# Optimization experiments

Measured on AMD Instinct MI355X. Metric: run time of the kernel, lower is better.

Reference implementation:

```python
import jax, jax.numpy as jnp
import numpy as np

H = 64
N_NODES = 12000
N_EDGES = 50000


def setup_inputs() -> dict:
    key = jax.random.key(0)
    ks = jax.random.split(key, 16)
    s = 1.0 / np.sqrt(H)
    inp = {
        "node": jax.random.normal(ks[0], (N_NODES, H), jnp.float32),
        "edge": jax.random.normal(ks[1], (N_EDGES, H), jnp.float32),
        "hidden_feats": jax.random.normal(ks[2], (N_NODES, H), jnp.float32),
        "src": jax.random.randint(ks[3], (N_EDGES,), 0, N_NODES, jnp.int32),
        "dst": jax.random.randint(ks[4], (N_EDGES,), 0, N_NODES, jnp.int32),
        # edge_network: Linear(H, 2H) -> ReLU -> Linear(2H, H*H)
        "W1": jax.random.uniform(ks[5], (2 * H, H), jnp.float32, -s, s),
        "b1": jax.random.uniform(ks[6], (2 * H,), jnp.float32, -s, s),
        "W2": jax.random.uniform(ks[7], (H * H, 2 * H), jnp.float32, -1 / np.sqrt(2 * H), 1 / np.sqrt(2 * H)),
        "b2": jax.random.uniform(ks[8], (H * H,), jnp.float32, -1 / np.sqrt(2 * H), 1 / np.sqrt(2 * H)),
        # GRUCell params (torch layout: [3H, H], gate order r,z,n)
        "W_ih": jax.random.uniform(ks[9], (3 * H, H), jnp.float32, -s, s),
        "W_hh": jax.random.uniform(ks[10], (3 * H, H), jnp.float32, -s, s),
        "b_ih": jax.random.uniform(ks[11], (3 * H,), jnp.float32, -s, s),
        "b_hh": jax.random.uniform(ks[12], (3 * H,), jnp.float32, -s, s),
        # LayerNorm params
        "gamma": jnp.ones((H,), jnp.float32),
        "beta": jnp.zeros((H,), jnp.float32),
    }
    return inp


def _gru_cell(x, h, W_ih, W_hh, b_ih, b_hh):
    gi = x @ W_ih.T + b_ih  # [N, 3H]
    gh = h @ W_hh.T + b_hh  # [N, 3H]
    r = jax.nn.sigmoid(gi[:, :H] + gh[:, :H])
    z = jax.nn.sigmoid(gi[:, H:2 * H] + gh[:, H:2 * H])
    n = jnp.tanh(gi[:, 2 * H:] + r * gh[:, 2 * H:])
    return (1.0 - z) * n + z * h


def reference(node, edge, hidden_feats, src, dst, W1, b1, W2, b2,
              W_ih, W_hh, b_ih, b_hh, gamma, beta):
    n_nodes = node.shape[0]
    # edge network -> per-edge [H,H] weight matrices
    eh = jax.nn.relu(edge @ W1.T + b1)                      # [E, 2H]
    Wedge = (eh @ W2.T + b2).reshape(-1, H, H)              # [E, H, H]
    # gather src feats, per-edge matmul (row-vector @ matrix), scatter-sum to dst
    msg = jnp.einsum('eh,ehk->ek', node[src], Wedge)        # [E, H]
    agg = jax.ops.segment_sum(msg, dst, num_segments=n_nodes)  # [N, H]
    new_node_feats = jax.nn.relu(agg)
    out = _gru_cell(new_node_feats, hidden_feats, W_ih, W_hh, b_ih, b_hh)
    # LayerNorm (eps=1e-5)
    mu = jnp.mean(out, axis=-1, keepdims=True)
    var = jnp.var(out, axis=-1, keepdims=True)
    out = (out - mu) * jax.lax.rsqrt(var + 1e-5) * gamma + beta
    return out
```

## Files before the change

### kernel.cpp

```cpp
#include <hip/hip_runtime.h>

#define H 64
#define NEDGE 50000
#define NNODE 12000
#define EPAD 50176

typedef _Float16 f16;
typedef _Float16 h8 __attribute__((ext_vector_type(8)));
typedef float f4 __attribute__((ext_vector_type(4)));
typedef float fv16 __attribute__((ext_vector_type(16)));

#define O_EDGEH 0ull
#define O_W2G   6422528ull
#define O_B2G   7471104ull
#define O_W1G   7479296ull
#define O_WG    7495680ull
#define O_AGG   7561216ull

__device__ __forceinline__ void async16(const void* g, void* l) {
  __builtin_amdgcn_global_load_lds((const __attribute__((address_space(1))) void*)g,
                                   (__attribute__((address_space(3))) void*)l, 16, 0, 0);
}

__device__ __forceinline__ fv16 zero16() {
  fv16 z;
#pragma unroll
  for (int i = 0; i < 16; ++i) z[i] = 0.f;
  return z;
}

__global__ __launch_bounds__(256) void k_prep(const float* __restrict__ edge, const float* __restrict__ W1,
                                              const float* __restrict__ W2, const float* __restrict__ b2,
                                              const float* __restrict__ Wih, const float* __restrict__ Whh,
                                              f16* __restrict__ edgeh, f16* __restrict__ w1g, f16* __restrict__ w2g,
                                              f16* __restrict__ b2g, f16* __restrict__ wg, float* __restrict__ agg) {
  int bid = blockIdx.x;
  int t = threadIdx.x;
  if (bid < 750) {
    int id = bid * 256 + t;
    *(f4*)(agg + (long)id * 4) = (f4){0.f, 0.f, 0.f, 0.f};
    return;
  }
  if (bid < 2318) {
    long id8 = (long)(bid - 750) * 256 + t;
    long e = id8 >> 3;
    int c = (int)(id8 & 7) * 8;
    h8 o = {};
    if (e < NEDGE) {
      const float* p = edge + e * 64 + c;
      f4 v0 = *(const f4*)p, v1 = *(const f4*)(p + 4);
#pragma unroll
      for (int j = 0; j < 4; ++j) { o[j] = (f16)v0[j]; o[4 + j] = (f16)v1[j]; }
    }
    *(h8*)(edgeh + e * 64 + c) = o;
    return;
  }
  if (bid < 4366) {
    int id = (bid - 2318) * 256 + t;
    int i = id & 7, l = (id >> 3) & 63, nh = (id >> 9) & 1, s = (id >> 10) & 7, h = id >> 13;
    int n = nh * 32 + (l & 31), j = s * 16 + ((l >> 5) << 3) + i;
    w2g[id] = (f16)W2[(h * 64 + n) * 128 + j];
    return;
  }
  if (bid < 4382) {
    int id = (bid - 4366) * 256 + t;
    int i = id & 7, l = (id >> 3) & 63, nh = (id >> 9) & 1, s = id >> 10;
    int n = nh * 32 + (l & 31), k = s * 16 + ((l >> 5) << 3) + i;
    b2g[id] = (f16)b2[k * 64 + n];
    return;
  }
  if (bid < 4414) {
    int id = (bid - 4382) * 256 + t;
    int i = id & 7, l = (id >> 3) & 63, nt = (id >> 9) & 3, s = id >> 11;
    int n = nt * 32 + (l & 31), k = s * 16 + ((l >> 5) << 3) + i;
    w1g[id] = (f16)W1[n * 64 + k];
    return;
  }
  {
    int id = (bid - 4414) * 256 + t;
    int ii = id & 7, l = (id >> 3) & 63, tt = (id >> 9) & 15, s = id >> 13;
    int k = s * 32 + ((l >> 4) << 3) + ii, n = tt * 16 + (l & 15);
    float v;
    if (n < 128) v = (k < 64) ? Wih[n * 64 + k] : Whh[n * 64 + (k - 64)];
    else if (n < 192) v = (k < 64) ? Wih[n * 64 + k] : 0.f;
    else v = (k < 64) ? 0.f : Whh[(n - 64) * 64 + (k - 64)];
    wg[id] = (f16)v;
  }
}

__global__ __launch_bounds__(256, 3) void k_msg(const float* __restrict__ node,
                                                const int* __restrict__ src, const int* __restrict__ dst,
                                                const f16* __restrict__ edgeh, const f16* __restrict__ w1g,
                                                const f16* __restrict__ w2g, const float* __restrict__ b1,
                                                float* __restrict__ agg) {
  __shared__ __align__(16) char lds[52736];
  f16* eh_s = (f16*)lds;
  char* bbuf = lds;
  f16* vT = (f16*)(lds + 32768);
  int* ssrc = (int*)(lds + 51200);
  int* sdst = (int*)(lds + 51712);
  float* b1s = (float*)(lds + 52224);

  int t = threadIdx.x;
  int e_base = blockIdx.x * 128;

  if (t < 128) {
    int eg = e_base + t;
    bool valid = eg < NEDGE;
    ssrc[t] = valid ? src[eg] : 0;
    sdst[t] = valid ? dst[eg] : 0;
  } else {
    b1s[t - 128] = b1[t - 128];
  }
  {
    int e = t >> 1, half = t & 1;
    int eg = e_base + e;
    int si = (eg < NEDGE) ? src[eg] : 0;
    const f4* nr = (const f4*)(node + (long)si * 64 + half * 32);
#pragma unroll
    for (int b = 0; b < 4; ++b) {
      f4 v0 = nr[b * 2], v1 = nr[b * 2 + 1];
      h8 pk;
#pragma unroll
      for (int m = 0; m < 4; ++m) { pk[m] = (f16)v0[m]; pk[4 + m] = (f16)v1[m]; }
      *(h8*)(vT + e * 72 + (half * 4 + b) * 8) = pk;
    }
  }
  __syncthreads();

  int wave = t >> 6, lane = t & 63;
  int wm = wave & 1, wn = wave >> 1;
  int l31 = lane & 31, lh = lane >> 5;

  {
    h8 afr[2][4];
#pragma unroll
    for (int mt = 0; mt < 2; ++mt)
#pragma unroll
      for (int s = 0; s < 4; ++s)
        afr[mt][s] = *(const h8*)(edgeh + (long)(e_base + wm * 64 + mt * 32 + l31) * 64 + s * 16 + lh * 8);
    h8 bfr[2][4];
#pragma unroll
    for (int nt = 0; nt < 2; ++nt)
#pragma unroll
      for (int s = 0; s < 4; ++s)
        bfr[nt][s] = *(const h8*)(w1g + ((s * 4 + wn * 2 + nt) * 64 + lane) * 8);
    fv16 acc_eh[2][2];
#pragma unroll
    for (int mt = 0; mt < 2; ++mt)
#pragma unroll
      for (int nt = 0; nt < 2; ++nt) acc_eh[mt][nt] = zero16();
#pragma unroll
    for (int s = 0; s < 4; ++s)
#pragma unroll
      for (int mt = 0; mt < 2; ++mt)
#pragma unroll
        for (int nt = 0; nt < 2; ++nt)
          acc_eh[mt][nt] = __builtin_amdgcn_mfma_f32_32x32x16_f16(afr[mt][s], bfr[nt][s], acc_eh[mt][nt], 0, 0, 0);
#pragma unroll
    for (int mt = 0; mt < 2; ++mt)
#pragma unroll
      for (int nt = 0; nt < 2; ++nt)
#pragma unroll
        for (int r = 0; r < 16; ++r) {
          int row = (r & 3) + 8 * (r >> 2) + 4 * lh;
          int e = wm * 64 + mt * 32 + row;
          int n = wn * 64 + nt * 32 + l31;
          float val = fmaxf(acc_eh[mt][nt][r] + b1s[n], 0.f);
          int o = n >> 3;
          eh_s[e * 128 + ((o ^ (e & 15)) << 3) + (n & 7)] = (f16)val;
        }
  }
  __syncthreads();

  h8 ehreg[2][8];
#pragma unroll
  for (int mt = 0; mt < 2; ++mt) {
    int e = wm * 64 + mt * 32 + l31;
#pragma unroll
    for (int s = 0; s < 8; ++s) {
      int o = (s * 2 + lh) ^ (e & 15);
      ehreg[mt][s] = *(const h8*)(eh_s + e * 128 + o * 8);
    }
  }
  __syncthreads();

  const char* w2b = (const char*)w2g;
#pragma unroll
  for (int r = 0; r < 4; ++r) async16(w2b + r * 4096 + t * 16, bbuf + r * 4096 + t * 16);

  fv16 acc[2];
  acc[0] = zero16(); acc[1] = zero16();
  const f16* vrow0 = vT + (wm * 64 + l31) * 72;
  const f16* vrow1 = vT + (wm * 64 + 32 + l31) * 72;

#pragma unroll 1
  for (int hb = 0; hb < 8; ++hb) {
    h8 vh0 = *(const h8*)(vrow0 + hb * 8);
    h8 vh1 = *(const h8*)(vrow1 + hb * 8);
#pragma unroll
    for (int hh = 0; hh < 8; ++hh) {
      int h = hb * 8 + hh;
      __syncthreads();
      {
        const char* gsrc = w2b + (long)(h + 1) * 16384;
        char* ldst = bbuf + ((h + 1) & 1) * 16384;
#pragma unroll
        for (int r = 0; r < 4; ++r) async16(gsrc + r * 4096 + t * 16, ldst + r * 4096 + t * 16);
      }
      const f16* bp = (const f16*)(bbuf + (h & 1) * 16384) + (wn * 64 + lane) * 8;
      f16 v0 = vh0[hh], v1 = vh1[hh];
#pragma unroll
      for (int s = 0; s < 8; ++s) {
        h8 bf = *(const h8*)(bp + s * 1024);
        h8 a0 = ehreg[0][s] * v0;
        acc[0] = __builtin_amdgcn_mfma_f32_32x32x16_f16(a0, bf, acc[0], 0, 0, 0);
        h8 a1 = ehreg[1][s] * v1;
        acc[1] = __builtin_amdgcn_mfma_f32_32x32x16_f16(a1, bf, acc[1], 0, 0, 0);
      }
    }
  }
  __syncthreads();
  {
    const f16* bp = (const f16*)bbuf + (wn * 64 + lane) * 8;
#pragma unroll
    for (int s = 0; s < 4; ++s) {
      h8 bf = *(const h8*)(bp + s * 1024);
      h8 a0 = *(const h8*)(vrow0 + (s * 2 + lh) * 8);
      h8 a1 = *(const h8*)(vrow1 + (s * 2 + lh) * 8);
      acc[0] = __builtin_amdgcn_mfma_f32_32x32x16_f16(a0, bf, acc[0], 0, 0, 0);
      acc[1] = __builtin_amdgcn_mfma_f32_32x32x16_f16(a1, bf, acc[1], 0, 0, 0);
    }
  }

  int n = wn * 32 + l31;
#pragma unroll
  for (int mt = 0; mt < 2; ++mt)
#pragma unroll
    for (int r = 0; r < 16; ++r) {
      int el = wm * 64 + mt * 32 + (r & 3) + 8 * (r >> 2) + 4 * lh;
      if (e_base + el < NEDGE)
        atomicAdd(&agg[(long)sdst[el] * 64 + n], acc[mt][r]);
    }
}

__global__ __launch_bounds__(256) void k_node(const float* __restrict__ agg, const float* __restrict__ hid,
                                              const f16* __restrict__ wg,
                                              const float* __restrict__ bih, const float* __restrict__ bhh,
                                              const float* __restrict__ gamma, const float* __restrict__ beta,
                                              float* __restrict__ out) {
  __shared__ __align__(16) f16 xh_s[128 * 136];
  __shared__ float bsum[128], bin_s[64], bhn_s[64], gam_s[64], bet_s[64];
  int t = threadIdx.x;
  int n0 = blockIdx.x * 128;

  if (t < 128) bsum[t] = bih[t] + bhh[t];
  else if (t < 192) bin_s[t - 128] = bih[t];
  else bhn_s[t - 192] = bhh[t - 64];
  if (t < 64) gam_s[t] = gamma[t];
  else if (t < 128) bet_s[t - 64] = beta[t - 64];

  {
    int m = t >> 1, half = t & 1;
    int mg = n0 + m;
    bool vld = mg < NNODE;
    const float* sp = half ? (hid + (long)mg * 64) : (agg + (long)mg * 64);
#pragma unroll
    for (int jj = 0; jj < 8; ++jj) {
      f4 v0 = {0, 0, 0, 0}, v1 = {0, 0, 0, 0};
      if (vld) { v0 = *(const f4*)(sp + jj * 8); v1 = *(const f4*)(sp + jj * 8 + 4); }
      h8 pk;
#pragma unroll
      for (int m2 = 0; m2 < 4; ++m2) {
        pk[m2] = (f16)(half ? v0[m2] : fmaxf(v0[m2], 0.f));
        pk[4 + m2] = (f16)(half ? v1[m2] : fmaxf(v1[m2], 0.f));
      }
      *(h8*)(xh_s + m * 136 + half * 64 + jj * 8) = pk;
    }
  }
  __syncthreads();

  int wave = t >> 6, lane = t & 63;
  int l15 = lane & 15, lq = lane >> 4;

  f4 acc[2][16];
#pragma unroll
  for (int g = 0; g < 2; ++g)
#pragma unroll
    for (int tt = 0; tt < 16; ++tt) acc[g][tt] = (f4){0.f, 0.f, 0.f, 0.f};

#pragma unroll
  for (int s = 0; s < 4; ++s) {
    h8 a0 = *(const h8*)(xh_s + (wave * 32 + l15) * 136 + s * 32 + lq * 8);
    h8 a1 = *(const h8*)(xh_s + (wave * 32 + 16 + l15) * 136 + s * 32 + lq * 8);
#pragma unroll
    for (int tt = 0; tt < 16; ++tt) {
      h8 b = *(const h8*)(wg + ((s * 16 + tt) * 64 + lane) * 8);
      acc[0][tt] = __builtin_amdgcn_mfma_f32_16x16x32_f16(a0, b, acc[0][tt], 0, 0, 0);
      acc[1][tt] = __builtin_amdgcn_mfma_f32_16x16x32_f16(a1, b, acc[1][tt], 0, 0, 0);
    }
  }

#pragma unroll
  for (int g = 0; g < 2; ++g)
#pragma unroll
    for (int r = 0; r < 4; ++r) {
      int mg = n0 + wave * 32 + g * 16 + lq * 4 + r;
      bool vld = mg < NNODE;
      float o[4], ssum = 0.f, s2 = 0.f;
#pragma unroll
      for (int t0 = 0; t0 < 4; ++t0) {
        int f = t0 * 16 + l15;
        float rpre = acc[g][t0][r] + bsum[f];
        float zpre = acc[g][4 + t0][r] + bsum[64 + f];
        float ginv = acc[g][8 + t0][r] + bin_s[f];
        float ghnv = acc[g][12 + t0][r] + bhn_s[f];
        float rr = 1.f / (1.f + __expf(-rpre));
        float zz = 1.f / (1.f + __expf(-zpre));
        float hv = vld ? hid[(long)mg * 64 + f] : 0.f;
        float nn = tanhf(ginv + rr * ghnv);
        float oo = (1.f - zz) * nn + zz * hv;
        o[t0] = oo; ssum += oo; s2 += oo * oo;
      }
#pragma unroll
      for (int d = 1; d < 16; d <<= 1) {
        ssum += __shfl_xor(ssum, d);
        s2 += __shfl_xor(s2, d);
      }
      float mu = ssum * (1.f / 64.f);
      float var = s2 * (1.f / 64.f) - mu * mu;
      float rstd = rsqrtf(var + 1e-5f);
      if (vld)
#pragma unroll
        for (int t0 = 0; t0 < 4; ++t0) {
          int f = t0 * 16 + l15;
          out[(long)mg * 64 + f] = (o[t0] - mu) * rstd * gam_s[f] + bet_s[f];
        }
    }
}

extern "C" void kernel_launch(void* const* d_in, const int* in_sizes, int n_in,
                              void* d_out, int out_size, void* d_ws, size_t ws_size,
                              hipStream_t stream) {
  const float* node = (const float*)d_in[0];
  const float* edge = (const float*)d_in[1];
  const float* hid = (const float*)d_in[2];
  const int* src = (const int*)d_in[3];
  const int* dst = (const int*)d_in[4];
  const float* W1 = (const float*)d_in[5];
  const float* b1 = (const float*)d_in[6];
  const float* W2 = (const float*)d_in[7];
  const float* b2 = (const float*)d_in[8];
  const float* Wih = (const float*)d_in[9];
  const float* Whh = (const float*)d_in[10];
  const float* bih = (const float*)d_in[11];
  const float* bhh = (const float*)d_in[12];
  const float* gamma = (const float*)d_in[13];
  const float* beta = (const float*)d_in[14];

  char* ws = (char*)d_ws;
  f16* edgeh = (f16*)(ws + O_EDGEH);
  f16* w2g = (f16*)(ws + O_W2G);
  f16* b2g = (f16*)(ws + O_B2G);
  f16* w1g = (f16*)(ws + O_W1G);
  f16* wg = (f16*)(ws + O_WG);
  float* agg = (float*)(ws + O_AGG);

  k_prep<<<4542, 256, 0, stream>>>(edge, W1, W2, b2, Wih, Whh, edgeh, w1g, w2g, b2g, wg, agg);
  k_msg<<<392, 256, 0, stream>>>(node, src, dst, edgeh, w1g, w2g, b1, agg);
  k_node<<<94, 256, 0, stream>>>(agg, hid, wg, bih, bhh, gamma, beta, (float*)d_out);
}
```

Baseline: 186.5 us.

## Fuse prep, message and node kernels into one persistent kernel with grid barriers

Merges the three launches into a single 392-block kernel. The prep work becomes grid-stride loops, and an atomic-counter grid barrier separates the prep, message and node phases. This removes two kernel launch gaps and the tail effects between dependent kernels. In exchange it relies on all 392 blocks being co-resident (launch bounds 256,2 across 256 CUs), which risks deadlock if occupancy is lower, and it adds a memset plus spin-wait costs.

```diff
diff --git a/kernel.cpp b/kernel.cpp
--- a/kernel.cpp
+++ b/kernel.cpp
@@ -1,9 +1,9 @@
 #include <hip/hip_runtime.h>
 
-#define H 64
 #define NEDGE 50000
 #define NNODE 12000
-#define EPAD 50176
+#define NB    392
+#define NT    100352
 
 typedef _Float16 f16;
 typedef _Float16 h8 __attribute__((ext_vector_type(8)));
@@ -16,6 +16,7 @@
 #define O_W1G   7479296ull
 #define O_WG    7495680ull
 #define O_AGG   7561216ull
+#define O_CNT   10633216ull
 
 __device__ __forceinline__ void async16(const void* g, void* l) {
   __builtin_amdgcn_global_load_lds((const __attribute__((address_space(1))) void*)g,
@@ -29,22 +30,38 @@
   return z;
 }
 
-__global__ __launch_bounds__(256) void k_prep(const float* __restrict__ edge, const float* __restrict__ W1,
-                                              const float* __restrict__ W2, const float* __restrict__ b2,
-                                              const float* __restrict__ Wih, const float* __restrict__ Whh,
-                                              f16* __restrict__ edgeh, f16* __restrict__ w1g, f16* __restrict__ w2g,
-                                              f16* __restrict__ b2g, f16* __restrict__ wg, float* __restrict__ agg) {
+__device__ __forceinline__ void gbar(int* cnt, int target) {
+  __syncthreads();
+  if (threadIdx.x == 0) {
+    __threadfence();
+    __hip_atomic_fetch_add(cnt, 1, __ATOMIC_ACQ_REL, __HIP_MEMORY_SCOPE_AGENT);
+    while (__hip_atomic_load(cnt, __ATOMIC_ACQUIRE, __HIP_MEMORY_SCOPE_AGENT) < target)
+      __builtin_amdgcn_s_sleep(2);
+  }
+  __syncthreads();
+}
+
+__global__ __launch_bounds__(256, 2) void k_fused(
+    const float* __restrict__ node, const float* __restrict__ edge, const float* __restrict__ hid,
+    const int* __restrict__ src, const int* __restrict__ dst,
+    const float* __restrict__ W1, const float* __restrict__ b1,
+    const float* __restrict__ W2, const float* __restrict__ b2,
+    const float* __restrict__ Wih, const float* __restrict__ Whh,
+    const float* __restrict__ bih, const float* __restrict__ bhh,
+    const float* __restrict__ gamma, const float* __restrict__ beta,
+    f16* __restrict__ edgeh, f16* __restrict__ w1g, f16* __restrict__ w2g,
+    f16* __restrict__ b2g, f16* __restrict__ wg, float* __restrict__ agg,
+    int* __restrict__ cnt, float* __restrict__ out) {
+  __shared__ __align__(16) char lds[52736];
+  int t = threadIdx.x;
   int bid = blockIdx.x;
-  int t = threadIdx.x;
-  if (bid < 750) {
-    int id = bid * 256 + t;
-    *(f4*)(agg + (long)id * 4) = (f4){0.f, 0.f, 0.f, 0.f};
-    return;
-  }
-  if (bid < 2318) {
-    long id8 = (long)(bid - 750) * 256 + t;
-    long e = id8 >> 3;
-    int c = (int)(id8 & 7) * 8;
+  int tid = bid * 256 + t;
+
+  for (int i = tid; i < 192000; i += NT)
+    ((f4*)agg)[i] = (f4){0.f, 0.f, 0.f, 0.f};
+  for (int i = tid; i < 401408; i += NT) {
+    long e = (long)i >> 3;
+    int c = (i & 7) * 8;
     h8 o = {};
     if (e < NEDGE) {
       const float* p = edge + e * 64 + c;
@@ -53,31 +70,23 @@
       for (int j = 0; j < 4; ++j) { o[j] = (f16)v0[j]; o[4 + j] = (f16)v1[j]; }
     }
     *(h8*)(edgeh + e * 64 + c) = o;
-    return;
-  }
-  if (bid < 4366) {
-    int id = (bid - 2318) * 256 + t;
+  }
+  for (int id = tid; id < 524288; id += NT) {
     int i = id & 7, l = (id >> 3) & 63, nh = (id >> 9) & 1, s = (id >> 10) & 7, h = id >> 13;
     int n = nh * 32 + (l & 31), j = s * 16 + ((l >> 5) << 3) + i;
     w2g[id] = (f16)W2[(h * 64 + n) * 128 + j];
-    return;
-  }
-  if (bid < 4382) {
-    int id = (bid - 4366) * 256 + t;
+  }
+  for (int id = tid; id < 4096; id += NT) {
     int i = id & 7, l = (id >> 3) & 63, nh = (id >> 9) & 1, s = id >> 10;
     int n = nh * 32 + (l & 31), k = s * 16 + ((l >> 5) << 3) + i;
     b2g[id] = (f16)b2[k * 64 + n];
-    return;
-  }
-  if (bid < 4414) {
-    int id = (bid - 4382) * 256 + t;
-    int i = id & 7, l = (id >> 3) & 63, nt = (id >> 9) & 3, s = id >> 11;
-    int n = nt * 32 + (l & 31), k = s * 16 + ((l >> 5) << 3) + i;
+  }
+  for (int id = tid; id < 8192; id += NT) {
+    int i = id & 7, l = (id >> 3) & 63, nt2 = (id >> 9) & 3, s = id >> 11;
+    int n = nt2 * 32 + (l & 31), k = s * 16 + ((l >> 5) << 3) + i;
     w1g[id] = (f16)W1[n * 64 + k];
-    return;
-  }
-  {
-    int id = (bid - 4414) * 256 + t;
+  }
+  for (int id = tid; id < 32768; id += NT) {
     int ii = id & 7, l = (id >> 3) & 63, tt = (id >> 9) & 15, s = id >> 13;
     int k = s * 32 + ((l >> 4) << 3) + ii, n = tt * 16 + (l & 15);
     float v;
@@ -86,257 +95,249 @@
     else v = (k < 64) ? 0.f : Whh[(n - 64) * 64 + (k - 64)];
     wg[id] = (f16)v;
   }
-}
-
-__global__ __launch_bounds__(256, 3) void k_msg(const float* __restrict__ node,
-                                                const int* __restrict__ src, const int* __restrict__ dst,
-                                                const f16* __restrict__ edgeh, const f16* __restrict__ w1g,
-                                                const f16* __restrict__ w2g, const float* __restrict__ b1,
-                                                float* __restrict__ agg) {
-  __shared__ __align__(16) char lds[52736];
-  f16* eh_s = (f16*)lds;
-  char* bbuf = lds;
-  f16* vT = (f16*)(lds + 32768);
-  int* ssrc = (int*)(lds + 51200);
-  int* sdst = (int*)(lds + 51712);
-  float* b1s = (float*)(lds + 52224);
-
-  int t = threadIdx.x;
-  int e_base = blockIdx.x * 128;
-
-  if (t < 128) {
-    int eg = e_base + t;
-    bool valid = eg < NEDGE;
-    ssrc[t] = valid ? src[eg] : 0;
-    sdst[t] = valid ? dst[eg] : 0;
-  } else {
-    b1s[t - 128] = b1[t - 128];
-  }
+  gbar(cnt, NB);
+
   {
-    int e = t >> 1, half = t & 1;
-    int eg = e_base + e;
-    int si = (eg < NEDGE) ? src[eg] : 0;
-    const f4* nr = (const f4*)(node + (long)si * 64 + half * 32);
-#pragma unroll
-    for (int b = 0; b < 4; ++b) {
-      f4 v0 = nr[b * 2], v1 = nr[b * 2 + 1];
-      h8 pk;
-#pragma unroll
-      for (int m = 0; m < 4; ++m) { pk[m] = (f16)v0[m]; pk[4 + m] = (f16)v1[m]; }
-      *(h8*)(vT + e * 72 + (half * 4 + b) * 8) = pk;
-    }
-  }
-  __syncthreads();
-
-  int wave = t >> 6, lane = t & 63;
-  int wm = wave & 1, wn = wave >> 1;
-  int l31 = lane & 31, lh = lane >> 5;
-
+    f16* eh_s = (f16*)lds;
+    char* bbuf = lds;
+    f16* vT = (f16*)(lds + 32768);
+    int* ssrc = (int*)(lds + 51200);
+    int* sdst = (int*)(lds + 51712);
+    float* b1s = (float*)(lds + 52224);
+    int e_base = bid * 128;
+
+    if (t < 128) {
+      int eg = e_base + t;
+      bool valid = eg < NEDGE;
+      ssrc[t] = valid ? src[eg] : 0;
+      sdst[t] = valid ? dst[eg] : 0;
+    } else {
+      b1s[t - 128] = b1[t - 128];
+    }
+    {
+      int e = t >> 1, half = t & 1;
+      int eg = e_base + e;
+      int si = (eg < NEDGE) ? src[eg] : 0;
+      const f4* nr = (const f4*)(node + (long)si * 64 + half * 32);
+#pragma unroll
+      for (int b = 0; b < 4; ++b) {
+        f4 v0 = nr[b * 2], v1 = nr[b * 2 + 1];
+        h8 pk;
+#pragma unroll
+        for (int m = 0; m < 4; ++m) { pk[m] = (f16)v0[m]; pk[4 + m] = (f16)v1[m]; }
+        *(h8*)(vT + e * 72 + (half * 4 + b) * 8) = pk;
+      }
+    }
+    __syncthreads();
+
+    int wave = t >> 6, lane = t & 63;
+    int wm = wave & 1, wn = wave >> 1;
+    int l31 = lane & 31, lh = lane >> 5;
+
+    {
+      h8 afr[2][4];
+#pragma unroll
+      for (int mt = 0; mt < 2; ++mt)
+#pragma unroll
+        for (int s = 0; s < 4; ++s)
+          afr[mt][s] = *(const h8*)(edgeh + (long)(e_base + wm * 64 + mt * 32 + l31) * 64 + s * 16 + lh * 8);
+      h8 bfr[2][4];
+#pragma unroll
+      for (int nt2 = 0; nt2 < 2; ++nt2)
+#pragma unroll
+        for (int s = 0; s < 4; ++s)
+          bfr[nt2][s] = *(const h8*)(w1g + ((s * 4 + wn * 2 + nt2) * 64 + lane) * 8);
+      fv16 acc_eh[2][2];
+#pragma unroll
+      for (int mt = 0; mt < 2; ++mt)
+#pragma unroll
+        for (int nt2 = 0; nt2 < 2; ++nt2) acc_eh[mt][nt2] = zero16();
+#pragma unroll
+      for (int s = 0; s < 4; ++s)
+#pragma unroll
+        for (int mt = 0; mt < 2; ++mt)
+#pragma unroll
+          for (int nt2 = 0; nt2 < 2; ++nt2)
+            acc_eh[mt][nt2] = __builtin_amdgcn_mfma_f32_32x32x16_f16(afr[mt][s], bfr[nt2][s], acc_eh[mt][nt2], 0, 0, 0);
+#pragma unroll
+      for (int mt = 0; mt < 2; ++mt)
+#pragma unroll
+        for (int nt2 = 0; nt2 < 2; ++nt2)
+#pragma unroll
+          for (int rr = 0; rr < 16; ++rr) {
+            int row = (rr & 3) + 8 * (rr >> 2) + 4 * lh;
+            int e = wm * 64 + mt * 32 + row;
+            int n = wn * 64 + nt2 * 32 + l31;
+            float val = fmaxf(acc_eh[mt][nt2][rr] + b1s[n], 0.f);
+            int o = n >> 3;
+            eh_s[e * 128 + ((o ^ (e & 15)) << 3) + (n & 7)] = (f16)val;
+          }
+    }
+    __syncthreads();
+
+    h8 ehreg[2][8];
+#pragma unroll
+    for (int mt = 0; mt < 2; ++mt) {
+      int e = wm * 64 + mt * 32 + l31;
+#pragma unroll
+      for (int s = 0; s < 8; ++s) {
+        int o = (s * 2 + lh) ^ (e & 15);
+        ehreg[mt][s] = *(const h8*)(eh_s + e * 128 + o * 8);
+      }
+    }
+    __syncthreads();
+
+    const char* w2b = (const char*)w2g;
+#pragma unroll
+    for (int r = 0; r < 4; ++r) async16(w2b + r * 4096 + t * 16, bbuf + r * 4096 + t * 16);
+
+    fv16 acc[2];
+    acc[0] = zero16(); acc[1] = zero16();
+    const f16* vrow0 = vT + (wm * 64 + l31) * 72;
+    const f16* vrow1 = vT + (wm * 64 + 32 + l31) * 72;
+
+#pragma unroll 1
+    for (int hb = 0; hb < 8; ++hb) {
+      h8 vh0 = *(const h8*)(vrow0 + hb * 8);
+      h8 vh1 = *(const h8*)(vrow1 + hb * 8);
+#pragma unroll
+      for (int hh = 0; hh < 8; ++hh) {
+        int h = hb * 8 + hh;
+        __syncthreads();
+        {
+          const char* gsrc = w2b + (long)(h + 1) * 16384;
+          char* ldst = bbuf + ((h + 1) & 1) * 16384;
+#pragma unroll
+          for (int r = 0; r < 4; ++r) async16(gsrc + r * 4096 + t * 16, ldst + r * 4096 + t * 16);
+        }
+        const f16* bp = (const f16*)(bbuf + (h & 1) * 16384) + (wn * 64 + lane) * 8;
+        f16 v0 = vh0[hh], v1 = vh1[hh];
+#pragma unroll
+        for (int s = 0; s < 8; ++s) {
+          h8 bf = *(const h8*)(bp + s * 1024);
+          h8 a0 = ehreg[0][s] * v0;
+          acc[0] = __builtin_amdgcn_mfma_f32_32x32x16_f16(a0, bf, acc[0], 0, 0, 0);
+          h8 a1 = ehreg[1][s] * v1;
+          acc[1] = __builtin_amdgcn_mfma_f32_32x32x16_f16(a1, bf, acc[1], 0, 0, 0);
+        }
+      }
+    }
+    __syncthreads();
+    {
+      const f16* bp = (const f16*)bbuf + (wn * 64 + lane) * 8;
+#pragma unroll
+      for (int s = 0; s < 4; ++s) {
+        h8 bf = *(const h8*)(bp + s * 1024);
+        h8 a0 = *(const h8*)(vrow0 + (s * 2 + lh) * 8);
+        h8 a1 = *(const h8*)(vrow1 + (s * 2 + lh) * 8);
+        acc[0] = __builtin_amdgcn_mfma_f32_32x32x16_f16(a0, bf, acc[0], 0, 0, 0);
+        acc[1] = __builtin_amdgcn_mfma_f32_32x32x16_f16(a1, bf, acc[1], 0, 0, 0);
+      }
+    }
+    int n = wn * 32 + l31;
+#pragma unroll
+    for (int mt = 0; mt < 2; ++mt)
+#pragma unroll
+      for (int r = 0; r < 16; ++r) {
+        int el = wm * 64 + mt * 32 + (r & 3) + 8 * (r >> 2) + 4 * lh;
+        if (e_base + el < NEDGE)
+          atomicAdd(&agg[(long)sdst[el] * 64 + n], acc[mt][r]);
+      }
+  }
+  gbar(cnt, 2 * NB);
+
+  if (bid >= 94) return;
   {
-    h8 afr[2][4];
-#pragma unroll
-    for (int mt = 0; mt < 2; ++mt)
-#pragma unroll
-      for (int s = 0; s < 4; ++s)
-        afr[mt][s] = *(const h8*)(edgeh + (long)(e_base + wm * 64 + mt * 32 + l31) * 64 + s * 16 + lh * 8);
-    h8 bfr[2][4];
-#pragma unroll
-    for (int nt = 0; nt < 2; ++nt)
-#pragma unroll
-      for (int s = 0; s < 4; ++s)
-        bfr[nt][s] = *(const h8*)(w1g + ((s * 4 + wn * 2 + nt) * 64 + lane) * 8);
-    fv16 acc_eh[2][2];
-#pragma unroll
-    for (int mt = 0; mt < 2; ++mt)
-#pragma unroll
-      for (int nt = 0; nt < 2; ++nt) acc_eh[mt][nt] = zero16();
-#pragma unroll
-    for (int s = 0; s < 4; ++s)
-#pragma unroll
-      for (int mt = 0; mt < 2; ++mt)
-#pragma unroll
-        for (int nt = 0; nt < 2; ++nt)
-          acc_eh[mt][nt] = __builtin_amdgcn_mfma_f32_32x32x16_f16(afr[mt][s], bfr[nt][s], acc_eh[mt][nt], 0, 0, 0);
-#pragma unroll
-    for (int mt = 0; mt < 2; ++mt)
-#pragma unroll
-      for (int nt = 0; nt < 2; ++nt)
-#pragma unroll
-        for (int r = 0; r < 16; ++r) {
-          int row = (r & 3) + 8 * (r >> 2) + 4 * lh;
-          int e = wm * 64 + mt * 32 + row;
-          int n = wn * 64 + nt * 32 + l31;
-          float val = fmaxf(acc_eh[mt][nt][r] + b1s[n], 0.f);
-          int o = n >> 3;
-          eh_s[e * 128 + ((o ^ (e & 15)) << 3) + (n & 7)] = (f16)val;
-        }
-  }
-  __syncthreads();
-
-  h8 ehreg[2][8];
-#pragma unroll
-  for (int mt = 0; mt < 2; ++mt) {
-    int e = wm * 64 + mt * 32 + l31;
-#pragma unroll
-    for (int s = 0; s < 8; ++s) {
-      int o = (s * 2 + lh) ^ (e & 15);
-      ehreg[mt][s] = *(const h8*)(eh_s + e * 128 + o * 8);
-    }
-  }
-  __syncthreads();
-
-  const char* w2b = (const char*)w2g;
-#pragma unroll
-  for (int r = 0; r < 4; ++r) async16(w2b + r * 4096 + t * 16, bbuf + r * 4096 + t * 16);
-
-  fv16 acc[2];
-  acc[0] = zero16(); acc[1] = zero16();
-  const f16* vrow0 = vT + (wm * 64 + l31) * 72;
-  const f16* vrow1 = vT + (wm * 64 + 32 + l31) * 72;
-
-#pragma unroll 1
-  for (int hb = 0; hb < 8; ++hb) {
-    h8 vh0 = *(const h8*)(vrow0 + hb * 8);
-    h8 vh1 = *(const h8*)(vrow1 + hb * 8);
-#pragma unroll
-    for (int hh = 0; hh < 8; ++hh) {
-      int h = hb * 8 + hh;
-      __syncthreads();
-      {
-        const char* gsrc = w2b + (long)(h + 1) * 16384;
-        char* ldst = bbuf + ((h + 1) & 1) * 16384;
-#pragma unroll
-        for (int r = 0; r < 4; ++r) async16(gsrc + r * 4096 + t * 16, ldst + r * 4096 + t * 16);
-      }
-      const f16* bp = (const f16*)(bbuf + (h & 1) * 16384) + (wn * 64 + lane) * 8;
-      f16 v0 = vh0[hh], v1 = vh1[hh];
-#pragma unroll
-      for (int s = 0; s < 8; ++s) {
-        h8 bf = *(const h8*)(bp + s * 1024);
-        h8 a0 = ehreg[0][s] * v0;
-        acc[0] = __builtin_amdgcn_mfma_f32_32x32x16_f16(a0, bf, acc[0], 0, 0, 0);
-        h8 a1 = ehreg[1][s] * v1;
-        acc[1] = __builtin_amdgcn_mfma_f32_32x32x16_f16(a1, bf, acc[1], 0, 0, 0);
-      }
-    }
-  }
-  __syncthreads();
-  {
-    const f16* bp = (const f16*)bbuf + (wn * 64 + lane) * 8;
+    f16* xh_s = (f16*)lds;
+    float* bsum = (float*)(lds + 34816);
+    float* bin_s = (float*)(lds + 35328);
+    float* bhn_s = (float*)(lds + 35584);
+    float* gam_s = (float*)(lds + 35840);
+    float* bet_s = (float*)(lds + 36096);
+    int n0 = bid * 128;
+
+    if (t < 128) bsum[t] = bih[t] + bhh[t];
+    else if (t < 192) bin_s[t - 128] = bih[t];
+    else bhn_s[t - 192] = bhh[t - 64];
+    if (t < 64) gam_s[t] = gamma[t];
+    else if (t < 128) bet_s[t - 64] = beta[t - 64];
+
+    {
+      int m = t >> 1, half = t & 1;
+      int mg = n0 + m;
+      bool vld = mg < NNODE;
+      const float* sp = half ? (hid + (long)mg * 64) : (agg + (long)mg * 64);
+#pragma unroll
+      for (int jj = 0; jj < 8; ++jj) {
+        f4 v0 = {0, 0, 0, 0}, v1 = {0, 0, 0, 0};
+        if (vld) { v0 = *(const f4*)(sp + jj * 8); v1 = *(const f4*)(sp + jj * 8 + 4); }
+        h8 pk;
+#pragma unroll
+        for (int m2 = 0; m2 < 4; ++m2) {
+          pk[m2] = (f16)(half ? v0[m2] : fmaxf(v0[m2], 0.f));
+          pk[4 + m2] = (f16)(half ? v1[m2] : fmaxf(v1[m2], 0.f));
+        }
+        *(h8*)(xh_s + m * 136 + half * 64 + jj * 8) = pk;
+      }
+    }
+    __syncthreads();
+
+    int wave = t >> 6, lane = t & 63;
+    int l15 = lane & 15, lq = lane >> 4;
+
+    f4 acc[2][16];
+#pragma unroll
+    for (int g = 0; g < 2; ++g)
+#pragma unroll
+      for (int tt = 0; tt < 16; ++tt) acc[g][tt] = (f4){0.f, 0.f, 0.f, 0.f};
 #pragma unroll
     for (int s = 0; s < 4; ++s) {
-      h8 bf = *(const h8*)(bp + s * 1024);
-      h8 a0 = *(const h8*)(vrow0 + (s * 2 + lh) * 8);
-      h8 a1 = *(const h8*)(vrow1 + (s * 2 + lh) * 8);
-      acc[0] = __builtin_amdgcn_mfma_f32_32x32x16_f16(a0, bf, acc[0], 0, 0, 0);
-      acc[1] = __builtin_amdgcn_mfma_f32_32x32x16_f16(a1, bf, acc[1], 0, 0, 0);
-    }
-  }
-
-  int n = wn * 32 + l31;
-#pragma unroll
-  for (int mt = 0; mt < 2; ++mt)
-#pragma unroll
-    for (int r = 0; r < 16; ++r) {
-      int el = wm * 64 + mt * 32 + (r & 3) + 8 * (r >> 2) + 4 * lh;
-      if (e_base + el < NEDGE)
-        atomicAdd(&agg[(long)sdst[el] * 64 + n], acc[mt][r]);
-    }
-}
-
-__global__ __launch_bounds__(256) void k_node(const float* __restrict__ agg, const float* __restrict__ hid,
-                                              const f16* __restrict__ wg,
-                                              const float* __restrict__ bih, const float* __restrict__ bhh,
-                                              const float* __restrict__ gamma, const float* __restrict__ beta,
-                                              float* __restrict__ out) {
-  __shared__ __align__(16) f16 xh_s[128 * 136];
-  __shared__ float bsum[128], bin_s[64], bhn_s[64], gam_s[64], bet_s[64];
-  int t = threadIdx.x;
-  int n0 = blockIdx.x * 128;
-
-  if (t < 128) bsum[t] = bih[t] + bhh[t];
-  else if (t < 192) bin_s[t - 128] = bih[t];
-  else bhn_s[t - 192] = bhh[t - 64];
-  if (t < 64) gam_s[t] = gamma[t];
-  else if (t < 128) bet_s[t - 64] = beta[t - 64];
-
-  {
-    int m = t >> 1, half = t & 1;
-    int mg = n0 + m;
-    bool vld = mg < NNODE;
-    const float* sp = half ? (hid + (long)mg * 64) : (agg + (long)mg * 64);
-#pragma unroll
-    for (int jj = 0; jj < 8; ++jj) {
-      f4 v0 = {0, 0, 0, 0}, v1 = {0, 0, 0, 0};
-      if (vld) { v0 = *(const f4*)(sp + jj * 8); v1 = *(const f4*)(sp + jj * 8 + 4); }
-      h8 pk;
-#pragma unroll
-      for (int m2 = 0; m2 < 4; ++m2) {
-        pk[m2] = (f16)(half ? v0[m2] : fmaxf(v0[m2], 0.f));
-        pk[4 + m2] = (f16)(half ? v1[m2] : fmaxf(v1[m2], 0.f));
-      }
-      *(h8*)(xh_s + m * 136 + half * 64 + jj * 8) = pk;
-    }
-  }
-  __syncthreads();
-
-  int wave = t >> 6, lane = t & 63;
-  int l15 = lane & 15, lq = lane >> 4;
-
-  f4 acc[2][16];
-#pragma unroll
-  for (int g = 0; g < 2; ++g)
-#pragma unroll
-    for (int tt = 0; tt < 16; ++tt) acc[g][tt] = (f4){0.f, 0.f, 0.f, 0.f};
-
-#pragma unroll
-  for (int s = 0; s < 4; ++s) {
-    h8 a0 = *(const h8*)(xh_s + (wave * 32 + l15) * 136 + s * 32 + lq * 8);
-    h8 a1 = *(const h8*)(xh_s + (wave * 32 + 16 + l15) * 136 + s * 32 + lq * 8);
-#pragma unroll
-    for (int tt = 0; tt < 16; ++tt) {
-      h8 b = *(const h8*)(wg + ((s * 16 + tt) * 64 + lane) * 8);
-      acc[0][tt] = __builtin_amdgcn_mfma_f32_16x16x32_f16(a0, b, acc[0][tt], 0, 0, 0);
-      acc[1][tt] = __builtin_amdgcn_mfma_f32_16x16x32_f16(a1, b, acc[1][tt], 0, 0, 0);
-    }
-  }
-
-#pragma unroll
-  for (int g = 0; g < 2; ++g)
-#pragma unroll
-    for (int r = 0; r < 4; ++r) {
-      int mg = n0 + wave * 32 + g * 16 + lq * 4 + r;
-      bool vld = mg < NNODE;
-      float o[4], ssum = 0.f, s2 = 0.f;
-#pragma unroll
-      for (int t0 = 0; t0 < 4; ++t0) {
-        int f = t0 * 16 + l15;
-        float rpre = acc[g][t0][r] + bsum[f];
-        float zpre = acc[g][4 + t0][r] + bsum[64 + f];
-        float ginv = acc[g][8 + t0][r] + bin_s[f];
-        float ghnv = acc[g][12 + t0][r] + bhn_s[f];
-        float rr = 1.f / (1.f + __expf(-rpre));
-        float zz = 1.f / (1.f + __expf(-zpre));
-        float hv = vld ? hid[(long)mg * 64 + f] : 0.f;
-        float nn = tanhf(ginv + rr * ghnv);
-        float oo = (1.f - zz) * nn + zz * hv;
-        o[t0] = oo; ssum += oo; s2 += oo * oo;
-      }
-#pragma unroll
-      for (int d = 1; d < 16; d <<= 1) {
-        ssum += __shfl_xor(ssum, d);
-        s2 += __shfl_xor(s2, d);
-      }
-      float mu = ssum * (1.f / 64.f);
-      float var = s2 * (1.f / 64.f) - mu * mu;
-      float rstd = rsqrtf(var + 1e-5f);
-      if (vld)
+      h8 a0 = *(const h8*)(xh_s + (wave * 32 + l15) * 136 + s * 32 + lq * 8);
+      h8 a1 = *(const h8*)(xh_s + (wave * 32 + 16 + l15) * 136 + s * 32 + lq * 8);
+#pragma unroll
+      for (int tt = 0; tt < 16; ++tt) {
+        h8 b = *(const h8*)(wg + ((s * 16 + tt) * 64 + lane) * 8);
+        acc[0][tt] = __builtin_amdgcn_mfma_f32_16x16x32_f16(a0, b, acc[0][tt], 0, 0, 0);
+        acc[1][tt] = __builtin_amdgcn_mfma_f32_16x16x32_f16(a1, b, acc[1][tt], 0, 0, 0);
+      }
+    }
+#pragma unroll
+    for (int g = 0; g < 2; ++g)
+#pragma unroll
+      for (int r = 0; r < 4; ++r) {
+        int mg = n0 + wave * 32 + g * 16 + lq * 4 + r;
+        bool vld = mg < NNODE;
+        float o[4], ssum = 0.f, s2 = 0.f;
 #pragma unroll
         for (int t0 = 0; t0 < 4; ++t0) {
           int f = t0 * 16 + l15;
-          out[(long)mg * 64 + f] = (o[t0] - mu) * rstd * gam_s[f] + bet_s[f];
-        }
-    }
+          float rpre = acc[g][t0][r] + bsum[f];
+          float zpre = acc[g][4 + t0][r] + bsum[64 + f];
+          float ginv = acc[g][8 + t0][r] + bin_s[f];
+          float ghnv = acc[g][12 + t0][r] + bhn_s[f];
+          float rr = 1.f / (1.f + __expf(-rpre));
+          float zz = 1.f / (1.f + __expf(-zpre));
+          float hv = vld ? hid[(long)mg * 64 + f] : 0.f;
+          float nn = tanhf(ginv + rr * ghnv);
+          float oo = (1.f - zz) * nn + zz * hv;
+          o[t0] = oo; ssum += oo; s2 += oo * oo;
+        }
+#pragma unroll
+        for (int d = 1; d < 16; d <<= 1) {
+          ssum += __shfl_xor(ssum, d);
+          s2 += __shfl_xor(s2, d);
+        }
+        float mu = ssum * (1.f / 64.f);
+        float var = s2 * (1.f / 64.f) - mu * mu;
+        float rstd = rsqrtf(var + 1e-5f);
+        if (vld)
+#pragma unroll
+          for (int t0 = 0; t0 < 4; ++t0) {
+            int f = t0 * 16 + l15;
+            out[(long)mg * 64 + f] = (o[t0] - mu) * rstd * gam_s[f] + bet_s[f];
+          }
+      }
+  }
 }
 
 extern "C" void kernel_launch(void* const* d_in, const int* in_sizes, int n_in,
@@ -365,8 +366,10 @@
   f16* w1g = (f16*)(ws + O_W1G);
   f16* wg = (f16*)(ws + O_WG);
   float* agg = (float*)(ws + O_AGG);
-
-  k_prep<<<4542, 256, 0, stream>>>(edge, W1, W2, b2, Wih, Whh, edgeh, w1g, w2g, b2g, wg, agg);
-  k_msg<<<392, 256, 0, stream>>>(node, src, dst, edgeh, w1g, w2g, b1, agg);
-  k_node<<<94, 256, 0, stream>>>(agg, hid, wg, bih, bhh, gamma, beta, (float*)d_out);
-}
+  int* cnt = (int*)(ws + O_CNT);
+
+  hipMemsetAsync(cnt, 0, 8, stream);
+  k_fused<<<NB, 256, 0, stream>>>(node, edge, hid, src, dst, W1, b1, W2, b2,
+                                  Wih, Whh, bih, bhh, gamma, beta,
+                                  edgeh, w1g, w2g, b2g, wg, agg, cnt, (float*)d_out);
+}
```

Result: slower. 313.0 us (+67.8%).
